# Optimization experiments

Measured on AMD Instinct MI355X. Metric: run time of the kernel, lower is better.

Reference implementation:

```python
import jax, jax.numpy as jnp
import numpy as np

K = 4096            # ca3_memory_slots
C = 2048            # ca3_code_dim
B = 8192            # query batch (episodes)
MAX_ITERS = 8       # cfg.pseudoinverse_iterations (spiking window T=8)
TOL = 1e-4          # cfg.convergence_tolerance
ALPHA_CLAMP = 5e-4  # torch.clamp(exp(log_scale), max=5e-4)


def setup_inputs() -> dict:
    key = jax.random.key(0)
    k1, k2, k3 = jax.random.split(key, 3)
    query = jax.random.normal(k1, (B, C), dtype=jnp.float32)
    # buffer init: torch.randn(K, C) * 0.01
    memory_mean = jax.random.normal(k2, (K, C), dtype=jnp.float32) * 0.01
    # nn.Parameter(torch.tensor(pseudoinverse_alpha_init)) -> scalar
    ben_israel_log_scale = jnp.float32(-0.5)
    return {"query": query, "memory_mean": memory_mean,
            "ben_israel_log_scale": ben_israel_log_scale}


def _ben_israel_pinv(A, log_scale):
    """Ben-Israel-Cohen iteration with masked early stopping (fixed trip count)."""
    A_fro_sq = jnp.sum(A * A)
    alpha = (1.0 / (A_fro_sq + 1e-8)) * jnp.minimum(jnp.exp(log_scale), ALPHA_CLAMP)
    pinv = alpha * A.T                       # (C, K)
    residual = jnp.array(jnp.inf, dtype=A.dtype)
    done = jnp.array(False)
    for _ in range(MAX_ITERS):
        pinv_new = 2.0 * pinv - pinv @ (A @ pinv)        # (C,K)
        recon = A @ (pinv_new @ A)                       # (K,C)
        res_new = jnp.linalg.norm(recon - A)             # Frobenius
        pinv = jnp.where(done, pinv, pinv_new)
        residual = jnp.where(done, residual, res_new)
        done = done | (res_new < TOL)
    return pinv, residual


def reference(query, memory_mean, ben_israel_log_scale):
    A = memory_mean                                      # (K, C)
    A_pinv, residual = _ben_israel_pinv(A, ben_israel_log_scale)  # (C, K)
    w = query @ A_pinv                                   # (B, K) addressing weights
    retrieved = w @ A                                    # (B, C) pattern completion
    return retrieved
```

## Files before the change

kernel.cpp:

```cpp
#include <hip/hip_runtime.h>
#include <hip/hip_bf16.h>
#include <cstdint>
#include <cstddef>


#define K_DIM 4096
#define C_DIM 2048
#define B_DIM 8192

typedef __bf16 bf16x8 __attribute__((ext_vector_type(8)));
typedef float f32x4 __attribute__((ext_vector_type(4)));

#define VMCNT(n) asm volatile("s_waitcnt vmcnt(" #n ")" ::: "memory")
#define LGKMCNT(n) asm volatile("s_waitcnt lgkmcnt(" #n ")" ::: "memory")
#define SBAR __builtin_amdgcn_s_barrier()
#define SCHED __builtin_amdgcn_sched_barrier(0)

__device__ __forceinline__ void async_load16(const void* g, void* l) {
  __builtin_amdgcn_global_load_lds(
      (const __attribute__((address_space(1))) void*)g,
      (__attribute__((address_space(3))) void*)l, 16, 0, 0);
}

__global__ __launch_bounds__(256) void prep_kernel(
    const float* __restrict__ A, __hip_bfloat16* __restrict__ At,
    const float* __restrict__ q, __hip_bfloat16* __restrict__ qb,
    float* __restrict__ wsf) {
  const int b = blockIdx.x;
  const int t = threadIdx.x;
  if (b < 2048) {
    __shared__ __align__(16) __hip_bfloat16 Ts[64 * 68];
    const int c0 = (b & 31) * 64;
    const int k0 = (b >> 5) * 64;
    const int c_l = t & 63;
    const int kq = t >> 6;
#pragma unroll
    for (int i = 0; i < 4; ++i) {
      int k_l = i * 16 + kq * 4;
      union { __hip_bfloat16 h[4]; uint2 u; } pk;
#pragma unroll
      for (int j = 0; j < 4; ++j)
        pk.h[j] = __float2bfloat16(A[(size_t)(k0 + k_l + j) * C_DIM + c0 + c_l]);
      *(uint2*)(Ts + c_l * 68 + k_l) = pk.u;
    }
    __syncthreads();
    const int c = t >> 2;
    const int seg = t & 3;
    const __hip_bfloat16* src = Ts + c * 68 + seg * 16;
    union { uint2 d[2]; uint4 qv; } o0, o1;
    o0.d[0] = *(const uint2*)(src + 0);
    o0.d[1] = *(const uint2*)(src + 4);
    o1.d[0] = *(const uint2*)(src + 8);
    o1.d[1] = *(const uint2*)(src + 12);
    __hip_bfloat16* dst = At + (size_t)(c0 + c) * K_DIM + k0 + seg * 16;
    *(uint4*)(dst + 0) = o0.qv;
    *(uint4*)(dst + 8) = o1.qv;
  } else {
    if (b == 2048 && t == 0) wsf[4] = 0.0f;
    const int n4 = B_DIM * C_DIM / 4;
    int tid = (b - 2048) * 256 + t;
    for (int i = tid; i < n4; i += 1024 * 256) {
      float4 v = ((const float4*)q)[i];
      __hip_bfloat16 o[4] = {__float2bfloat16(v.x), __float2bfloat16(v.y),
                             __float2bfloat16(v.z), __float2bfloat16(v.w)};
      *(uint2*)(qb + 4 * (size_t)i) = *(const uint2*)o;
    }
  }
}

__global__ __launch_bounds__(256, 2) void gemm_m(
    const __hip_bfloat16* __restrict__ At, __hip_bfloat16* __restrict__ Mb,
    float* __restrict__ wsf) {
  constexpr int BK = 64;
  constexpr int NT = K_DIM / BK;
  __shared__ __align__(16) __hip_bfloat16 As[2][128 * BK];
  __shared__ __align__(16) __hip_bfloat16 Bs[2][128 * BK];
  const int tid = threadIdx.x;
  const int wave = tid >> 6, lane = tid & 63;
  const int tile_m = blockIdx.y * 128, tile_n = blockIdx.x * 128;
  const int wm = (wave >> 1) * 64, wn = (wave & 1) * 64;
  const int lr = lane >> 3, lcl = (lane & 7) ^ lr;
  const __hip_bfloat16* aB = At + (size_t)(tile_m + wave * 32 + lr) * K_DIM + lcl * 8;
  const __hip_bfloat16* bB = At + (size_t)(tile_n + wave * 32 + lr) * K_DIM + lcl * 8;
  const int l15 = lane & 15, lg = lane >> 4, l7 = lane & 7;
  f32x4 acc[4][4] = {};

#pragma unroll
  for (int c = 0; c < 4; ++c) {
    async_load16(aB + (size_t)(c * 8) * K_DIM, &As[0][(wave * 32 + c * 8) * BK]);
    async_load16(bB + (size_t)(c * 8) * K_DIM, &Bs[0][(wave * 32 + c * 8) * BK]);
  }
  VMCNT(0);
  SBAR;

  for (int t = 0; t < NT; ++t) {
    const int buf = t & 1;
    if (t + 1 < NT) {
#pragma unroll
      for (int c = 0; c < 4; ++c) {
        async_load16(aB + (size_t)(c * 8) * K_DIM + (size_t)(t + 1) * BK,
                     &As[buf ^ 1][(wave * 32 + c * 8) * BK]);
        async_load16(bB + (size_t)(c * 8) * K_DIM + (size_t)(t + 1) * BK,
                     &Bs[buf ^ 1][(wave * 32 + c * 8) * BK]);
      }
      VMCNT(8);
    } else {
      VMCNT(0);
    }
    SBAR;
#pragma unroll
    for (int kh = 0; kh < 2; ++kh) {
      bf16x8 a[4], bb[4];
#pragma unroll
      for (int f = 0; f < 4; ++f) {
        a[f]  = *(const bf16x8*)&As[buf][(wm + f * 16 + l15) * BK + (((kh * 4 + lg) ^ l7) * 8)];
        bb[f] = *(const bf16x8*)&Bs[buf][(wn + f * 16 + l15) * BK + (((kh * 4 + lg) ^ l7) * 8)];
      }
      __builtin_amdgcn_s_setprio(1);
#pragma unroll
      for (int f = 0; f < 4; ++f)
#pragma unroll
        for (int j = 0; j < 4; ++j)
          acc[f][j] = __builtin_amdgcn_mfma_f32_16x16x32_bf16(a[f], bb[j], acc[f][j], 0, 0, 0);
      __builtin_amdgcn_s_setprio(0);
    }
    SBAR;
  }

  float tsum = 0.0f;
  const bool dg = (tile_m == tile_n) && (wm == wn) && (lg == (l15 >> 2));
#pragma unroll
  for (int f = 0; f < 4; ++f) {
    const int gm = tile_m + wm + f * 16 + lg * 4;
#pragma unroll
    for (int j = 0; j < 4; ++j) {
      const int gn = tile_n + wn + j * 16 + l15;
#pragma unroll
      for (int r = 0; r < 4; ++r) {
        Mb[(size_t)(gm + r) * C_DIM + gn] = __float2bfloat16(acc[f][j][r]);
        if (f == j && r == (l15 & 3) && dg) tsum += acc[f][j][r];
      }
    }
  }
  if (dg) atomicAdd(wsf + 4, tsum);
}

__global__ __launch_bounds__(512, 2) void gemm_qm(
    const __hip_bfloat16* __restrict__ Ab, const __hip_bfloat16* __restrict__ Bb,
    float* __restrict__ Fp, const float* __restrict__ ls,
    const float* __restrict__ wsf) {
  constexpr int BK = 64;
  constexpr int NT = C_DIM / BK;
  __shared__ __align__(16) __hip_bfloat16 As[2][256 * BK];
  __shared__ __align__(16) __hip_bfloat16 Bs[2][256 * BK];
  const int tid = threadIdx.x;
  const int wave = tid >> 6, lane = tid & 63;
  const int tile_m = blockIdx.y * 256, tile_n = blockIdx.x * 256;
  const int wm = (wave >> 2) * 128, wn = (wave & 3) * 64;
  const int lr = lane >> 3, lcl = (lane & 7) ^ lr;
  const __hip_bfloat16* aBase = Ab + (size_t)(tile_m + wave * 16 + lr) * C_DIM + lcl * 8;
  const __hip_bfloat16* bBase = Bb + (size_t)(tile_n + wave * 16 + lr) * C_DIM + lcl * 8;
  const int l15 = lane & 15, lg = lane >> 4, l7 = lane & 7;

  bf16x8 a0[4], a1[4], b0[4], b1[4];
  f32x4 acc[8][4] = {};

  auto stA = [&](int buf, int h, int t) {
    const __hip_bfloat16* s = aBase + (size_t)(h * 128) * C_DIM + (size_t)t * BK;
    __hip_bfloat16* d = &As[buf][(h * 128 + wave * 16) * BK];
    async_load16(s, d);
    async_load16(s + (size_t)8 * C_DIM, d + 8 * BK);
  };
  auto stB = [&](int buf, int h, int t) {
    const __hip_bfloat16* s = bBase + (size_t)(h * 128) * C_DIM + (size_t)t * BK;
    __hip_bfloat16* d = &Bs[buf][(h * 128 + wave * 16) * BK];
    async_load16(s, d);
    async_load16(s + (size_t)8 * C_DIM, d + 8 * BK);
  };
  auto rdA = [&](int buf, int mh, int kh, bf16x8* dst) {
    const __hip_bfloat16* p =
        &As[buf][(wm + mh * 64 + l15) * BK + (((kh * 4 + lg) ^ l7) * 8)];
#pragma unroll
    for (int f = 0; f < 4; ++f) dst[f] = *(const bf16x8*)(p + f * 16 * BK);
  };
  auto rdB = [&](int buf, int kh, bf16x8* dst) {
    const __hip_bfloat16* p =
        &Bs[buf][(wn + l15) * BK + (((kh * 4 + lg) ^ l7) * 8)];
#pragma unroll
    for (int f = 0; f < 4; ++f) dst[f] = *(const bf16x8*)(p + f * 16 * BK);
  };
  auto mm = [&](int mh, const bf16x8* a, const bf16x8* b) {
    __builtin_amdgcn_s_setprio(1);
#pragma unroll
    for (int f = 0; f < 4; ++f)
#pragma unroll
      for (int j = 0; j < 4; ++j)
        acc[mh * 4 + f][j] = __builtin_amdgcn_mfma_f32_16x16x32_bf16(
            a[f], b[j], acc[mh * 4 + f][j], 0, 0, 0);
    __builtin_amdgcn_s_setprio(0);
  };

  stA(0, 0, 0); stA(0, 1, 0);
  stB(0, 0, 0); stB(0, 1, 0);
  stB(1, 0, 1); stB(1, 1, 1);
  VMCNT(4);
  SBAR;
  rdA(0, 0, 0, a0);
  rdB(0, 0, b0);

  for (int t = 0; t < NT; ++t) {
    const int buf = t & 1;
    rdA(buf, 1, 0, a1);
    rdB(buf, 1, b1);
    if (t + 1 < NT) stA(buf ^ 1, 0, t + 1);
    SCHED; SBAR; SCHED;
    mm(0, a0, b0);
    SBAR;
    rdA(buf, 0, 1, a0);
    if (t + 1 < NT) stA(buf ^ 1, 1, t + 1);
    LGKMCNT(4);
    SCHED; SBAR; SCHED;
    mm(1, a1, b0);
    SBAR;
    rdA(buf, 1, 1, a1);
    if (t + 2 < NT) {
      stB(buf, 0, t + 2);
      VMCNT(2);
    } else {
      VMCNT(0);
    }
    SCHED; SBAR; SCHED;
    mm(0, a0, b1);
    SBAR;
    if (t + 1 < NT) {
      rdA(buf ^ 1, 0, 0, a0);
      rdB(buf ^ 1, 0, b0);
      if (t + 2 < NT) stB(buf, 1, t + 2);
    }
    SCHED; SBAR; SCHED;
    mm(1, a1, b1);
    SBAR;
  }

  const float c1 = 256.0f * fminf(expf(ls[0]), 5e-4f) / (wsf[4] + 1e-8f);
#pragma unroll
  for (int m = 0; m < 8; ++m) {
    const int gm = tile_m + wm + m * 16 + lg * 4;
#pragma unroll
    for (int j = 0; j < 4; ++j) {
      const int gn = tile_n + wn + j * 16 + l15;
#pragma unroll
      for (int r = 0; r < 4; ++r)
        Fp[(size_t)(gm + r) * C_DIM + gn] = c1 * acc[m][j][r];
    }
  }
}

extern "C" void kernel_launch(void* const* d_in, const int* in_sizes, int n_in,
                              void* d_out, int out_size, void* d_ws, size_t ws_size,
                              hipStream_t stream) {
  const float* query = (const float*)d_in[0];
  const float* A = (const float*)d_in[1];
  const float* ls = (const float*)d_in[2];
  float* out = (float*)d_out;

  char* ws = (char*)d_ws;
  float* wsf = (float*)ws;
  size_t off = 256;
  __hip_bfloat16* At = (__hip_bfloat16*)(ws + off);
  off += (size_t)C_DIM * K_DIM * 2;
  __hip_bfloat16* qb = (__hip_bfloat16*)(ws + off);
  off += (size_t)B_DIM * C_DIM * 2;
  __hip_bfloat16* Mb = (__hip_bfloat16*)(ws + off);

  prep_kernel<<<3072, 256, 0, stream>>>(A, At, query, qb, wsf);
  gemm_m<<<dim3(16, 16), 256, 0, stream>>>(At, Mb, wsf);
  gemm_qm<<<dim3(8, 32), 512, 0, stream>>>(qb, Mb, out, ls, wsf);
}
```

Before: 289.8 us.

## Split-K the Gram GEMM with a reduce kernel and restructure QM pipeline

The A^T A Gram GEMM now splits the K dimension four ways across blockIdx.z, writing fp32 partials into the output buffer, which serves as scratch. A new reduce kernel sums the partials, converts them to bf16 and accumulates the trace. The aim is to fill the GPU: the old 256-block grid underused the CUs. The Gram kernel also drops double buffering in favour of a single buffer with __syncthreads, and the main QM GEMM loop is rewritten into four quarter-steps with a simpler register and barrier schedule. The costs are extra fp32 partial traffic, one more launch, and a possibly less overlapped QM main loop.

```diff
diff --git a/kernel.cpp b/kernel.cpp
--- a/kernel.cpp
+++ b/kernel.cpp
@@ -7,14 +7,15 @@
 #define K_DIM 4096
 #define C_DIM 2048
 #define B_DIM 8192
+#define SPLITK 4
+#define KCHUNK (K_DIM / SPLITK)
 
 typedef __bf16 bf16x8 __attribute__((ext_vector_type(8)));
 typedef float f32x4 __attribute__((ext_vector_type(4)));
 
 #define VMCNT(n) asm volatile("s_waitcnt vmcnt(" #n ")" ::: "memory")
-#define LGKMCNT(n) asm volatile("s_waitcnt lgkmcnt(" #n ")" ::: "memory")
+#define LGKMCNT0 asm volatile("s_waitcnt lgkmcnt(0)" ::: "memory")
 #define SBAR __builtin_amdgcn_s_barrier()
-#define SCHED __builtin_amdgcn_sched_barrier(0)
 
 __device__ __forceinline__ void async_load16(const void* g, void* l) {
   __builtin_amdgcn_global_load_lds(
@@ -68,67 +69,57 @@
   }
 }
 
-__global__ __launch_bounds__(256, 2) void gemm_m(
-    const __hip_bfloat16* __restrict__ At, __hip_bfloat16* __restrict__ Mb,
-    float* __restrict__ wsf) {
+__global__ __launch_bounds__(256, 4) void gemm_m(
+    const __hip_bfloat16* __restrict__ At, float* __restrict__ P) {
   constexpr int BK = 64;
-  constexpr int NT = K_DIM / BK;
-  __shared__ __align__(16) __hip_bfloat16 As[2][128 * BK];
-  __shared__ __align__(16) __hip_bfloat16 Bs[2][128 * BK];
+  constexpr int NT = KCHUNK / BK;
+  __shared__ __align__(16) __hip_bfloat16 As[128 * BK];
+  __shared__ __align__(16) __hip_bfloat16 Bs[128 * BK];
   const int tid = threadIdx.x;
   const int wave = tid >> 6, lane = tid & 63;
   const int tile_m = blockIdx.y * 128, tile_n = blockIdx.x * 128;
+  const int kstart = blockIdx.z * KCHUNK;
   const int wm = (wave >> 1) * 64, wn = (wave & 1) * 64;
   const int lr = lane >> 3, lcl = (lane & 7) ^ lr;
-  const __hip_bfloat16* aB = At + (size_t)(tile_m + wave * 32 + lr) * K_DIM + lcl * 8;
-  const __hip_bfloat16* bB = At + (size_t)(tile_n + wave * 32 + lr) * K_DIM + lcl * 8;
+  const __hip_bfloat16* aB =
+      At + (size_t)(tile_m + wave * 32 + lr) * K_DIM + kstart + lcl * 8;
+  const __hip_bfloat16* bB =
+      At + (size_t)(tile_n + wave * 32 + lr) * K_DIM + kstart + lcl * 8;
   const int l15 = lane & 15, lg = lane >> 4, l7 = lane & 7;
   f32x4 acc[4][4] = {};
 
-#pragma unroll
-  for (int c = 0; c < 4; ++c) {
-    async_load16(aB + (size_t)(c * 8) * K_DIM, &As[0][(wave * 32 + c * 8) * BK]);
-    async_load16(bB + (size_t)(c * 8) * K_DIM, &Bs[0][(wave * 32 + c * 8) * BK]);
-  }
-  VMCNT(0);
-  SBAR;
-
   for (int t = 0; t < NT; ++t) {
-    const int buf = t & 1;
-    if (t + 1 < NT) {
-#pragma unroll
-      for (int c = 0; c < 4; ++c) {
-        async_load16(aB + (size_t)(c * 8) * K_DIM + (size_t)(t + 1) * BK,
-                     &As[buf ^ 1][(wave * 32 + c * 8) * BK]);
-        async_load16(bB + (size_t)(c * 8) * K_DIM + (size_t)(t + 1) * BK,
-                     &Bs[buf ^ 1][(wave * 32 + c * 8) * BK]);
-      }
-      VMCNT(8);
-    } else {
-      VMCNT(0);
-    }
-    SBAR;
+#pragma unroll
+    for (int c = 0; c < 4; ++c) {
+      async_load16(aB + (size_t)(c * 8) * K_DIM + (size_t)t * BK,
+                   &As[(wave * 32 + c * 8) * BK]);
+      async_load16(bB + (size_t)(c * 8) * K_DIM + (size_t)t * BK,
+                   &Bs[(wave * 32 + c * 8) * BK]);
+    }
+    __syncthreads();
 #pragma unroll
     for (int kh = 0; kh < 2; ++kh) {
       bf16x8 a[4], bb[4];
 #pragma unroll
       for (int f = 0; f < 4; ++f) {
-        a[f]  = *(const bf16x8*)&As[buf][(wm + f * 16 + l15) * BK + (((kh * 4 + lg) ^ l7) * 8)];
-        bb[f] = *(const bf16x8*)&Bs[buf][(wn + f * 16 + l15) * BK + (((kh * 4 + lg) ^ l7) * 8)];
+        a[f]  = *(const bf16x8*)&As[(wm + f * 16 + l15) * BK +
+                                    (((kh * 4 + lg) ^ l7) * 8)];
+        bb[f] = *(const bf16x8*)&Bs[(wn + f * 16 + l15) * BK +
+                                    (((kh * 4 + lg) ^ l7) * 8)];
       }
       __builtin_amdgcn_s_setprio(1);
 #pragma unroll
       for (int f = 0; f < 4; ++f)
 #pragma unroll
         for (int j = 0; j < 4; ++j)
-          acc[f][j] = __builtin_amdgcn_mfma_f32_16x16x32_bf16(a[f], bb[j], acc[f][j], 0, 0, 0);
+          acc[f][j] = __builtin_amdgcn_mfma_f32_16x16x32_bf16(
+              a[f], bb[j], acc[f][j], 0, 0, 0);
       __builtin_amdgcn_s_setprio(0);
     }
-    SBAR;
-  }
-
-  float tsum = 0.0f;
-  const bool dg = (tile_m == tile_n) && (wm == wn) && (lg == (l15 >> 2));
+    __syncthreads();
+  }
+
+  float* Pz = P + (size_t)blockIdx.z * C_DIM * C_DIM;
 #pragma unroll
   for (int f = 0; f < 4; ++f) {
     const int gm = tile_m + wm + f * 16 + lg * 4;
@@ -136,13 +127,38 @@
     for (int j = 0; j < 4; ++j) {
       const int gn = tile_n + wn + j * 16 + l15;
 #pragma unroll
-      for (int r = 0; r < 4; ++r) {
-        Mb[(size_t)(gm + r) * C_DIM + gn] = __float2bfloat16(acc[f][j][r]);
-        if (f == j && r == (l15 & 3) && dg) tsum += acc[f][j][r];
-      }
-    }
-  }
-  if (dg) atomicAdd(wsf + 4, tsum);
+      for (int r = 0; r < 4; ++r)
+        Pz[(size_t)(gm + r) * C_DIM + gn] = acc[f][j][r];
+    }
+  }
+}
+
+__global__ __launch_bounds__(256) void reduce4_kernel(
+    const float* __restrict__ P, __hip_bfloat16* __restrict__ Mb,
+    float* __restrict__ wsf) {
+  const size_t CC = (size_t)C_DIM * C_DIM;
+  const int n4 = (int)(CC / 4);
+  int tid = blockIdx.x * blockDim.x + threadIdx.x;
+  int stride = gridDim.x * blockDim.x;
+  float tsum = 0.0f;
+  for (int i = tid; i < n4; i += stride) {
+    float4 a = ((const float4*)P)[i];
+#pragma unroll
+    for (int z = 1; z < SPLITK; ++z) {
+      float4 b = *(const float4*)(P + z * CC + (size_t)i * 4);
+      a.x += b.x; a.y += b.y; a.z += b.z; a.w += b.w;
+    }
+    __hip_bfloat16 o[4] = {__float2bfloat16(a.x), __float2bfloat16(a.y),
+                           __float2bfloat16(a.z), __float2bfloat16(a.w)};
+    *(uint2*)(Mb + 4 * (size_t)i) = *(const uint2*)o;
+    const float av[4] = {a.x, a.y, a.z, a.w};
+#pragma unroll
+    for (int j = 0; j < 4; ++j) {
+      int e = 4 * i + j;
+      if (e % (C_DIM + 1) == 0) tsum += av[j];
+    }
+  }
+  if (tsum != 0.0f) atomicAdd(wsf + 4, tsum);
 }
 
 __global__ __launch_bounds__(512, 2) void gemm_qm(
@@ -158,12 +174,11 @@
   const int tile_m = blockIdx.y * 256, tile_n = blockIdx.x * 256;
   const int wm = (wave >> 2) * 128, wn = (wave & 3) * 64;
   const int lr = lane >> 3, lcl = (lane & 7) ^ lr;
-  const __hip_bfloat16* aBase = Ab + (size_t)(tile_m + wave * 16 + lr) * C_DIM + lcl * 8;
-  const __hip_bfloat16* bBase = Bb + (size_t)(tile_n + wave * 16 + lr) * C_DIM + lcl * 8;
+  const __hip_bfloat16* aBase =
+      Ab + (size_t)(tile_m + wave * 16 + lr) * C_DIM + lcl * 8;
+  const __hip_bfloat16* bBase =
+      Bb + (size_t)(tile_n + wave * 16 + lr) * C_DIM + lcl * 8;
   const int l15 = lane & 15, lg = lane >> 4, l7 = lane & 7;
-
-  bf16x8 a0[4], a1[4], b0[4], b1[4];
-  f32x4 acc[8][4] = {};
 
   auto stA = [&](int buf, int h, int t) {
     const __hip_bfloat16* s = aBase + (size_t)(h * 128) * C_DIM + (size_t)t * BK;
@@ -177,69 +192,60 @@
     async_load16(s, d);
     async_load16(s + (size_t)8 * C_DIM, d + 8 * BK);
   };
-  auto rdA = [&](int buf, int mh, int kh, bf16x8* dst) {
-    const __hip_bfloat16* p =
-        &As[buf][(wm + mh * 64 + l15) * BK + (((kh * 4 + lg) ^ l7) * 8)];
-#pragma unroll
-    for (int f = 0; f < 4; ++f) dst[f] = *(const bf16x8*)(p + f * 16 * BK);
-  };
-  auto rdB = [&](int buf, int kh, bf16x8* dst) {
-    const __hip_bfloat16* p =
-        &Bs[buf][(wn + l15) * BK + (((kh * 4 + lg) ^ l7) * 8)];
-#pragma unroll
-    for (int f = 0; f < 4; ++f) dst[f] = *(const bf16x8*)(p + f * 16 * BK);
-  };
-  auto mm = [&](int mh, const bf16x8* a, const bf16x8* b) {
-    __builtin_amdgcn_s_setprio(1);
-#pragma unroll
-    for (int f = 0; f < 4; ++f)
-#pragma unroll
-      for (int j = 0; j < 4; ++j)
-        acc[mh * 4 + f][j] = __builtin_amdgcn_mfma_f32_16x16x32_bf16(
-            a[f], b[j], acc[mh * 4 + f][j], 0, 0, 0);
-    __builtin_amdgcn_s_setprio(0);
-  };
+
+  f32x4 acc[8][4] = {};
 
   stA(0, 0, 0); stA(0, 1, 0);
   stB(0, 0, 0); stB(0, 1, 0);
   stB(1, 0, 1); stB(1, 1, 1);
   VMCNT(4);
   SBAR;
-  rdA(0, 0, 0, a0);
-  rdB(0, 0, b0);
 
   for (int t = 0; t < NT; ++t) {
     const int buf = t & 1;
-    rdA(buf, 1, 0, a1);
-    rdB(buf, 1, b1);
-    if (t + 1 < NT) stA(buf ^ 1, 0, t + 1);
-    SCHED; SBAR; SCHED;
-    mm(0, a0, b0);
-    SBAR;
-    rdA(buf, 0, 1, a0);
-    if (t + 1 < NT) stA(buf ^ 1, 1, t + 1);
-    LGKMCNT(4);
-    SCHED; SBAR; SCHED;
-    mm(1, a1, b0);
-    SBAR;
-    rdA(buf, 1, 1, a1);
-    if (t + 2 < NT) {
-      stB(buf, 0, t + 2);
-      VMCNT(2);
-    } else {
-      VMCNT(0);
-    }
-    SCHED; SBAR; SCHED;
-    mm(0, a0, b1);
-    SBAR;
-    if (t + 1 < NT) {
-      rdA(buf ^ 1, 0, 0, a0);
-      rdB(buf ^ 1, 0, b0);
-      if (t + 2 < NT) stB(buf, 1, t + 2);
-    }
-    SCHED; SBAR; SCHED;
-    mm(1, a1, b1);
-    SBAR;
+    bf16x8 breg[4][2];
+#pragma unroll
+    for (int q = 0; q < 4; ++q) {
+      bf16x8 af[2][2];
+#pragma unroll
+      for (int f = 0; f < 2; ++f)
+#pragma unroll
+        for (int s = 0; s < 2; ++s)
+          af[f][s] = *(const bf16x8*)&As[buf][(wm + q * 32 + f * 16 + l15) * BK +
+                                             ((((s << 2) | lg) ^ l7) << 3)];
+      if (q == 0) {
+#pragma unroll
+        for (int j = 0; j < 4; ++j)
+#pragma unroll
+          for (int s = 0; s < 2; ++s)
+            breg[j][s] = *(const bf16x8*)&Bs[buf][(wn + j * 16 + l15) * BK +
+                                                 ((((s << 2) | lg) ^ l7) << 3)];
+      }
+      if (q == 0 && t + 1 < NT) stA(buf ^ 1, 0, t + 1);
+      if (q == 1 && t + 1 < NT) stA(buf ^ 1, 1, t + 1);
+      if (q == 2 && t + 2 < NT) stB(buf, 0, t + 2);
+      if (q == 3) {
+        if (t + 2 < NT) {
+          stB(buf, 1, t + 2);
+          VMCNT(4);
+        } else {
+          VMCNT(0);
+        }
+      }
+      SBAR;
+      LGKMCNT0;
+      __builtin_amdgcn_s_setprio(1);
+#pragma unroll
+      for (int s = 0; s < 2; ++s)
+#pragma unroll
+        for (int f = 0; f < 2; ++f)
+#pragma unroll
+          for (int j = 0; j < 4; ++j)
+            acc[q * 2 + f][j] = __builtin_amdgcn_mfma_f32_16x16x32_bf16(
+                af[f][s], breg[j][s], acc[q * 2 + f][j], 0, 0, 0);
+      __builtin_amdgcn_s_setprio(0);
+      SBAR;
+    }
   }
 
   const float c1 = 256.0f * fminf(expf(ls[0]), 5e-4f) / (wsf[4] + 1e-8f);
@@ -273,7 +279,10 @@
   off += (size_t)B_DIM * C_DIM * 2;
   __hip_bfloat16* Mb = (__hip_bfloat16*)(ws + off);
 
+  float* P = out;
+
   prep_kernel<<<3072, 256, 0, stream>>>(A, At, query, qb, wsf);
-  gemm_m<<<dim3(16, 16), 256, 0, stream>>>(At, Mb, wsf);
-  gemm_qm<<<dim3(8, 32), 512, 0, stream>>>(qb, Mb, out, ls, wsf);
-}
+  gemm_m<<<dim3(C_DIM / 128, C_DIM / 128, SPLITK), 256, 0, stream>>>(At, P);
+  reduce4_kernel<<<1024, 256, 0, stream>>>(P, Mb, wsf);
+  gemm_qm<<<dim3(C_DIM / 256, B_DIM / 256), 512, 0, stream>>>(qb, Mb, out, ls, wsf);
+}
```

Measured after the change: 305.1 us. 5.3% more time.
